# Performance work log

Hardware: AMD Instinct MI355X
Metric: run time of the kernel (lower is better)

The kernel has to match this reference:

```python
import jax, jax.numpy as jnp
import numpy as np
import math

H = 16
D_MODEL = 1024
D_K = D_MODEL // H  # 64
B = 4
S = 2048
D_V = 64


def setup_inputs() -> dict:
    key0 = jax.random.key(0)
    ks = jax.random.split(key0, 7)
    scale = 1.0 / math.sqrt(D_MODEL)
    return {
        "query": jax.random.normal(ks[0], (B, S, D_MODEL), jnp.float32),
        "key": jax.random.normal(ks[1], (B, S, D_MODEL), jnp.float32),
        "value": jax.random.normal(ks[2], (B, D_V, S), jnp.float32),
        "Wq": jax.random.normal(ks[3], (D_MODEL, D_MODEL), jnp.float32) * scale,
        "bq": jax.random.normal(ks[4], (D_MODEL,), jnp.float32) * scale,
        "Wk": jax.random.normal(ks[5], (D_MODEL, D_MODEL), jnp.float32) * scale,
        "bk": jax.random.normal(ks[6], (D_MODEL,), jnp.float32) * scale,
    }


def reference(query, key, value, Wq, bq, Wk, bk):
    nb = query.shape[0]
    # Linear projections then split heads: [B,S,d_model] -> [B,h,S,d_k]
    q = (query @ Wq.T + bq).reshape(nb, -1, H, D_K).transpose(0, 2, 1, 3)
    k = (key @ Wk.T + bk).reshape(nb, -1, H, D_K).transpose(0, 2, 1, 3)
    # value.repeat(h,1,1,1).permute(1,0,3,2): [B,dv,Sk] -> broadcast over heads
    # with last two axes swapped -> effectively v[b,s,d] = value[b,d,s]
    v = jnp.swapaxes(value, 1, 2)  # [B, Sk, dv]
    # Scaled dot-product attention (mask branch is a no-op: m == zeros)
    scores = jnp.einsum("bhqd,bhkd->bhqk", q, k) / math.sqrt(D_K)
    p_attn = jax.nn.softmax(scores, axis=-1)
    # value identical across heads, contract directly with base v
    x = jnp.einsum("bhqk,bkd->bhqd", p_attn, v)  # [B,h,Sq,dv]
    return (jnp.mean(x, axis=1), q)
```

## Files before the change

kernel.cpp:

```cpp
#include <hip/hip_runtime.h>


typedef unsigned short u16;
typedef __attribute__((ext_vector_type(8))) u16 u16x8;
typedef __attribute__((ext_vector_type(8))) __bf16 bf16x8;
typedef __attribute__((ext_vector_type(4))) float f32x4;
typedef __attribute__((ext_vector_type(16))) float f32x16;
typedef __attribute__((ext_vector_type(2))) unsigned u32x2;
typedef __attribute__((ext_vector_type(4))) unsigned u32x4;

typedef const __attribute__((address_space(1))) void gvoid;
typedef __attribute__((address_space(3))) void lvoid;

__device__ __forceinline__ void gload16(const void* g, void* l) {
  __builtin_amdgcn_global_load_lds((gvoid*)g, (lvoid*)l, 16, 0, 0);
}

__device__ __forceinline__ u16 f2bf(float f) {
  unsigned u = __builtin_bit_cast(unsigned, f);
  u += 0x7fffu + ((u >> 16) & 1u);
  return (u16)(u >> 16);
}

__device__ __forceinline__ unsigned cvtpk(float lo, float hi) {
  unsigned r;
  asm("v_cvt_pk_bf16_f32 %0, %1, %2" : "=v"(r) : "v"(lo), "v"(hi));
  return r;
}

__device__ __forceinline__ float exp2a(float x) {
  float r;
  asm("v_exp_f32 %0, %1" : "=v"(r) : "v"(x));
  return r;
}

__device__ __forceinline__ f32x16 zero16() {
  f32x16 z;
#pragma unroll
  for (int i = 0; i < 16; ++i) z[i] = 0.f;
  return z;
}

__global__ void cvt_small(const float* __restrict__ wq, const float* __restrict__ wk,
                          const float* __restrict__ v,
                          u16* __restrict__ wqb, u16* __restrict__ wkb, u16* __restrict__ vb) {
  int i = blockIdx.x * 256 + threadIdx.x;
  const float* s;
  u16* d;
  int off;
  if (i < 262144)      { s = wq; d = wqb; off = i; }
  else if (i < 524288) { s = wk; d = wkb; off = i - 262144; }
  else if (i < 655360) { s = v;  d = vb;  off = i - 524288; }
  else return;
  float4 x = reinterpret_cast<const float4*>(s)[off];
  ushort4 o;
  o.x = f2bf(x.x); o.y = f2bf(x.y); o.z = f2bf(x.z); o.w = f2bf(x.w);
  reinterpret_cast<ushort4*>(d)[off] = o;
}

__global__ __launch_bounds__(256) void proj_gemm(
    const float* __restrict__ qf, const float* __restrict__ kf,
    const u16* __restrict__ Wqb, const u16* __restrict__ Wkb,
    const float* __restrict__ bq, const float* __restrict__ bk,
    float* __restrict__ out1, u16* __restrict__ k_ws)
{
  const int z = blockIdx.z;
  const float* __restrict__ A = z ? kf : qf;
  const u16* __restrict__ W = z ? Wkb : Wqb;
  const float* __restrict__ bias = z ? bk : bq;

  __shared__ u16 As[2][128 * 64];
  __shared__ u16 Bs[2][128 * 64];

  const int tid = threadIdx.x;
  const int lane = tid & 63;
  const int w = tid >> 6;
  const int ln = lane & 15;
  const int lh = lane >> 4;
  const int wm = w >> 1, wn = w & 1;
  const int n0 = blockIdx.x * 128;
  const int j0 = blockIdx.y * 128;

  f32x4 acc[4][4];
#pragma unroll
  for (int mt = 0; mt < 4; ++mt)
#pragma unroll
    for (int nt = 0; nt < 4; ++nt)
      acc[mt][nt] = f32x4{0.f, 0.f, 0.f, 0.f};

  const int r_ = tid >> 3, c8_ = tid & 7;

#pragma unroll
  for (int it = 0; it < 4; ++it) {
    int r = it * 32 + r_;
    gload16(&W[(size_t)(j0 + r) * 1024 + c8_ * 8], &Bs[0][(it * 256 + w * 64) * 8]);
  }
#pragma unroll
  for (int j = 0; j < 4; ++j) {
    int u = tid + j * 256;
    int r = u >> 3, c8 = (u & 7) * 8;
    const float* s = &A[(size_t)(n0 + r) * 1024 + c8];
    float4 x0 = *reinterpret_cast<const float4*>(s);
    float4 x1 = *reinterpret_cast<const float4*>(s + 4);
    u32x4 wv{cvtpk(x0.x, x0.y), cvtpk(x0.z, x0.w), cvtpk(x1.x, x1.y), cvtpk(x1.z, x1.w)};
    *reinterpret_cast<u32x4*>(&As[0][r * 64 + c8]) = wv;
  }
  __syncthreads();

  for (int kt = 0; kt < 16; ++kt) {
    const int cur = kt & 1, nb = cur ^ 1;
    float4 ax0[4], ax1[4];
    if (kt < 15) {
#pragma unroll
      for (int it = 0; it < 4; ++it) {
        int r = it * 32 + r_;
        gload16(&W[(size_t)(j0 + r) * 1024 + (kt + 1) * 64 + c8_ * 8],
                &Bs[nb][(it * 256 + w * 64) * 8]);
      }
#pragma unroll
      for (int j = 0; j < 4; ++j) {
        int u = tid + j * 256;
        int r = u >> 3, c8 = (u & 7) * 8;
        const float* s = &A[(size_t)(n0 + r) * 1024 + (kt + 1) * 64 + c8];
        ax0[j] = *reinterpret_cast<const float4*>(s);
        ax1[j] = *reinterpret_cast<const float4*>(s + 4);
      }
    }
#pragma unroll
    for (int ks = 0; ks < 2; ++ks) {
      bf16x8 a[4], bfr[4];
#pragma unroll
      for (int mt = 0; mt < 4; ++mt)
        a[mt] = __builtin_bit_cast(bf16x8,
            *reinterpret_cast<const u16x8*>(&As[cur][(wm * 64 + mt * 16 + ln) * 64 + lh * 8 + ks * 32]));
#pragma unroll
      for (int nt = 0; nt < 4; ++nt)
        bfr[nt] = __builtin_bit_cast(bf16x8,
            *reinterpret_cast<const u16x8*>(&Bs[cur][(wn * 64 + nt * 16 + ln) * 64 + lh * 8 + ks * 32]));
      __builtin_amdgcn_s_setprio(1);
#pragma unroll
      for (int mt = 0; mt < 4; ++mt)
#pragma unroll
        for (int nt = 0; nt < 4; ++nt)
          acc[mt][nt] = __builtin_amdgcn_mfma_f32_16x16x32_bf16(a[mt], bfr[nt], acc[mt][nt], 0, 0, 0);
      __builtin_amdgcn_s_setprio(0);
    }
    if (kt < 15) {
#pragma unroll
      for (int j = 0; j < 4; ++j) {
        int u = tid + j * 256;
        int r = u >> 3, c8 = (u & 7) * 8;
        u32x4 wv{cvtpk(ax0[j].x, ax0[j].y), cvtpk(ax0[j].z, ax0[j].w),
                 cvtpk(ax1[j].x, ax1[j].y), cvtpk(ax1[j].z, ax1[j].w)};
        *reinterpret_cast<u32x4*>(&As[nb][r * 64 + c8]) = wv;
      }
      __syncthreads();
    }
  }

#pragma unroll
  for (int nt = 0; nt < 4; ++nt) {
    int j = j0 + wn * 64 + nt * 16 + ln;
    float bv = bias[j];
    int h = j >> 6, d = j & 63;
#pragma unroll
    for (int mt = 0; mt < 4; ++mt) {
#pragma unroll
      for (int r = 0; r < 4; ++r) {
        int n = n0 + wm * 64 + mt * 16 + lh * 4 + r;
        int bidx = n >> 11, s = n & 2047;
        size_t off = ((size_t)(bidx * 16 + h) * 2048 + s) * 64 + d;
        float val = acc[mt][nt][r] + bv;
        if (z == 0) out1[off] = val;
        else        k_ws[off] = f2bf(val);
      }
    }
  }
}

#define SOFTMAX_CVT(P, PF0, PF1, LACC)                                               \
  {                                                                                  \
    _Pragma("unroll")                                                                \
    for (int r = 0; r < 16; ++r) P[r] = exp2a(P[r]);                                 \
    LACC += (((P[0]+P[1])+(P[2]+P[3])) + ((P[4]+P[5])+(P[6]+P[7])))                  \
          + (((P[8]+P[9])+(P[10]+P[11])) + ((P[12]+P[13])+(P[14]+P[15])));           \
    u32x2 sA0 = __builtin_amdgcn_permlane32_swap(cvtpk(P[0],P[1]),   cvtpk(P[4],P[5]),   false,false); \
    u32x2 sB0 = __builtin_amdgcn_permlane32_swap(cvtpk(P[2],P[3]),   cvtpk(P[6],P[7]),   false,false); \
    u32x2 sA1 = __builtin_amdgcn_permlane32_swap(cvtpk(P[8],P[9]),   cvtpk(P[12],P[13]), false,false); \
    u32x2 sB1 = __builtin_amdgcn_permlane32_swap(cvtpk(P[10],P[11]), cvtpk(P[14],P[15]), false,false); \
    u32x4 w0_{sA0[0], sB0[0], sA0[1], sB0[1]};                                       \
    u32x4 w1_{sA1[0], sB1[0], sA1[1], sB1[1]};                                       \
    PF0 = __builtin_bit_cast(bf16x8, w0_);                                           \
    PF1 = __builtin_bit_cast(bf16x8, w1_);                                           \
  }

#define ST_BLOCK(ST)                                                                 \
  {                                                                                  \
    f32x16 p = zero16();                                                             \
    __builtin_amdgcn_s_setprio(1);                                                   \
    _Pragma("unroll")                                                                \
    for (int c = 0; c < 4; ++c) {                                                    \
      int ka = bo + ((((ST * 32 + l31) * 128) + c * 32 + hi * 16) ^ xm);             \
      bf16x8 kf = __builtin_bit_cast(bf16x8, *reinterpret_cast<const u16x8*>(KtB + ka)); \
      p = __builtin_amdgcn_mfma_f32_32x32x16_bf16(kf, aq[c], p, 0, 0, 0);            \
    }                                                                                \
    __builtin_amdgcn_s_setprio(0);                                                   \
    bf16x8 pf0, pf1;                                                                 \
    SOFTMAX_CVT(p, pf0, pf1, lA);                                                    \
    _Pragma("unroll")                                                                \
    for (int kc = 0; kc < 2; ++kc) {                                                 \
      int cb = ST * 64 + kc * 32 + hi * 16;                                          \
      bf16x8 vA = __builtin_bit_cast(bf16x8,                                         \
          *reinterpret_cast<const u16x8*>(VtB + bo + ((l31 * 128 + cb) ^ xm)));      \
      bf16x8 vB = __builtin_bit_cast(bf16x8,                                         \
          *reinterpret_cast<const u16x8*>(VtB + bo + (((32 + l31) * 128 + cb) ^ xm))); \
      bf16x8 pf = kc ? pf1 : pf0;                                                    \
      __builtin_amdgcn_s_setprio(1);                                                 \
      oA = __builtin_amdgcn_mfma_f32_32x32x16_bf16(vA, pf, oA, 0, 0, 0);             \
      oB = __builtin_amdgcn_mfma_f32_32x32x16_bf16(vB, pf, oB, 0, 0, 0);             \
      __builtin_amdgcn_s_setprio(0);                                                 \
    }                                                                                \
  }

__global__ __launch_bounds__(256, 4) void attn_kernel(
    const float* __restrict__ qf, const u16* __restrict__ k_ws,
    const u16* __restrict__ valb, u16* __restrict__ x_ws)
{
  const int wgid = (blockIdx.x & 7) * 128 + (blockIdx.x >> 3);
  const int qblk = wgid & 15;
  const int h = (wgid >> 4) & 15;
  const int b = wgid >> 8;
  const int bh = b * 16 + h;

  const int tid = threadIdx.x, lane = tid & 63, w = tid >> 6;
  const int l31 = lane & 31, hi = lane >> 5;
  const int xm = (lane & 7) << 4;

  __shared__ u16 Kt[2][4096];
  __shared__ u16 Vt[2][4096];
  char* KtB = (char*)&Kt[0][0];
  char* VtB = (char*)&Vt[0][0];

  bf16x8 aq[4];
  {
    const float qs = 0.125f * 1.4426950408889634f;
    const size_t qb0 = ((size_t)bh * 2048 + qblk * 128 + w * 32 + l31) * 64;
#pragma unroll
    for (int c = 0; c < 4; ++c) {
      const float* src = &qf[qb0 + c * 16 + hi * 8];
      float4 v0 = *reinterpret_cast<const float4*>(src);
      float4 v1 = *reinterpret_cast<const float4*>(src + 4);
      u16x8 t;
      t[0] = f2bf(v0.x * qs); t[1] = f2bf(v0.y * qs);
      t[2] = f2bf(v0.z * qs); t[3] = f2bf(v0.w * qs);
      t[4] = f2bf(v1.x * qs); t[5] = f2bf(v1.y * qs);
      t[6] = f2bf(v1.z * qs); t[7] = f2bf(v1.w * qs);
      aq[c] = __builtin_bit_cast(bf16x8, t);
    }
  }

  const u16* kg = k_ws + (size_t)bh * 131072;
  const u16* vg = valb + (size_t)b * 131072;
  const int u0 = tid, u1 = tid + 256;
  const u16* ks0 = kg + (u0 >> 3) * 64 + ((u0 ^ (u0 >> 3)) & 7) * 8;
  const u16* ks1 = kg + (u1 >> 3) * 64 + ((u1 ^ (u1 >> 3)) & 7) * 8;
  const u16* vs0 = vg + (u0 >> 3) * 2048 + ((u0 ^ (u0 >> 3)) & 7) * 8;
  const u16* vs1 = vg + (u1 >> 3) * 2048 + ((u1 ^ (u1 >> 3)) & 7) * 8;
  u16* kd0 = &Kt[0][(w * 64) * 8];
  u16* kd1 = &Kt[0][(256 + w * 64) * 8];
  u16* vd0 = &Vt[0][(w * 64) * 8];
  u16* vd1 = &Vt[0][(256 + w * 64) * 8];

  gload16(ks0, kd0); gload16(ks1, kd1);
  gload16(vs0, vd0); gload16(vs1, vd1);

  float lA = 0.0f;
  f32x16 oA = zero16(), oB = zero16();
  int cur = 0;
  __syncthreads();

  for (int t = 0; t < 32; ++t) {
    if (t < 31) {
      int nb = (cur ^ 1) * 4096;
      size_t ko = (size_t)(t + 1) * 4096;
      int vo = (t + 1) * 64;
      gload16(ks0 + ko, kd0 + nb); gload16(ks1 + ko, kd1 + nb);
      gload16(vs0 + vo, vd0 + nb); gload16(vs1 + vo, vd1 + nb);
    }
    const int bo = cur * 8192;

    ST_BLOCK(0)
    ST_BLOCK(1)

    __syncthreads();
    cur ^= 1;
  }

  float lr = lA + __shfl_xor(lA, 32);
  float inv = 1.0f / lr;
  size_t ob0 = ((size_t)bh * 2048 + qblk * 128 + w * 32 + l31) * 64;
#pragma unroll
  for (int g = 0; g < 4; ++g) {
    u32x2 aa{cvtpk(oA[g*4+0]*inv, oA[g*4+1]*inv), cvtpk(oA[g*4+2]*inv, oA[g*4+3]*inv)};
    u32x2 bb{cvtpk(oB[g*4+0]*inv, oB[g*4+1]*inv), cvtpk(oB[g*4+2]*inv, oB[g*4+3]*inv)};
    *reinterpret_cast<u32x2*>(&x_ws[ob0 + g * 8 + hi * 4]) = aa;
    *reinterpret_cast<u32x2*>(&x_ws[ob0 + 32 + g * 8 + hi * 4]) = bb;
  }
}

__global__ void mean_heads(const u16* __restrict__ x_ws, float* __restrict__ out0) {
  int i = blockIdx.x * 256 + threadIdx.x;
  int d0 = (i & 7) * 8;
  int s = (i >> 3) & 2047;
  int b = i >> 14;
  float acc[8];
#pragma unroll
  for (int j = 0; j < 8; ++j) acc[j] = 0.f;
#pragma unroll
  for (int h = 0; h < 16; ++h) {
    u16x8 v = *reinterpret_cast<const u16x8*>(
        &x_ws[(((size_t)(b * 16 + h) * 2048 + s) << 6) + d0]);
#pragma unroll
    for (int j = 0; j < 8; ++j)
      acc[j] += __builtin_bit_cast(float, (unsigned)v[j] << 16);
  }
  float4 o0{acc[0] * 0.0625f, acc[1] * 0.0625f, acc[2] * 0.0625f, acc[3] * 0.0625f};
  float4 o1{acc[4] * 0.0625f, acc[5] * 0.0625f, acc[6] * 0.0625f, acc[7] * 0.0625f};
  size_t ob = ((size_t)(b * 2048 + s) << 6) + d0;
  *reinterpret_cast<float4*>(&out0[ob]) = o0;
  *reinterpret_cast<float4*>(&out0[ob + 4]) = o1;
}

extern "C" void kernel_launch(void* const* d_in, const int* in_sizes, int n_in,
                              void* d_out, int out_size, void* d_ws, size_t ws_size,
                              hipStream_t stream) {
  (void)in_sizes; (void)n_in; (void)out_size; (void)ws_size;
  const float* query = (const float*)d_in[0];
  const float* key   = (const float*)d_in[1];
  const float* value = (const float*)d_in[2];
  const float* Wq    = (const float*)d_in[3];
  const float* bq    = (const float*)d_in[4];
  const float* Wk    = (const float*)d_in[5];
  const float* bk    = (const float*)d_in[6];

  float* out0 = (float*)d_out;
  float* out1 = out0 + 524288;

  char* ws = (char*)d_ws;
  const size_t MB = 1u << 20;
  u16* x_ws = (u16*)(ws + 0);
  u16* Wqb  = (u16*)(ws + 32 * MB);
  u16* Wkb  = (u16*)(ws + 34 * MB);
  u16* valb = (u16*)(ws + 36 * MB);
  u16* k_ws = (u16*)(ws + 37 * MB);

  cvt_small<<<2560, 256, 0, stream>>>(Wq, Wk, value, Wqb, Wkb, valb);
  proj_gemm<<<dim3(64, 8, 2), 256, 0, stream>>>(query, key, Wqb, Wkb, bq, bk, out1, k_ws);
  attn_kernel<<<1024, 256, 0, stream>>>(out1, k_ws, valb, x_ws);
  mean_heads<<<256, 256, 0, stream>>>(x_ws, out0);
}
```

Measured before the change: 154.7 us.

## Load projection A operand straight into registers and swizzle the weight tile in LDS

The fp32 activation tile is no longer staged and converted through shared memory. Each lane now loads its MFMA fragment directly from global memory and converts it to bf16 in registers, which removes the As buffer and its LDS writes. The weight tile in LDS gets an XOR swizzle on its 16-byte chunks to reduce bank conflicts on fragment reads. The trade-off is that the activation loads are no longer prefetched a stage ahead: they are issued just before the MFMAs and fetched redundantly by the two column-warps, so memory latency may be exposed.

```diff
diff --git a/kernel.cpp b/kernel.cpp
--- a/kernel.cpp
+++ b/kernel.cpp
@@ -69,7 +69,6 @@
   const u16* __restrict__ W = z ? Wkb : Wqb;
   const float* __restrict__ bias = z ? bk : bq;
 
-  __shared__ u16 As[2][128 * 64];
   __shared__ u16 Bs[2][128 * 64];
 
   const int tid = threadIdx.x;
@@ -88,55 +87,43 @@
     for (int nt = 0; nt < 4; ++nt)
       acc[mt][nt] = f32x4{0.f, 0.f, 0.f, 0.f};
 
-  const int r_ = tid >> 3, c8_ = tid & 7;
-
-#pragma unroll
-  for (int it = 0; it < 4; ++it) {
-    int r = it * 32 + r_;
-    gload16(&W[(size_t)(j0 + r) * 1024 + c8_ * 8], &Bs[0][(it * 256 + w * 64) * 8]);
-  }
-#pragma unroll
-  for (int j = 0; j < 4; ++j) {
-    int u = tid + j * 256;
-    int r = u >> 3, c8 = (u & 7) * 8;
-    const float* s = &A[(size_t)(n0 + r) * 1024 + c8];
-    float4 x0 = *reinterpret_cast<const float4*>(s);
-    float4 x1 = *reinterpret_cast<const float4*>(s + 4);
-    u32x4 wv{cvtpk(x0.x, x0.y), cvtpk(x0.z, x0.w), cvtpk(x1.x, x1.y), cvtpk(x1.z, x1.w)};
-    *reinterpret_cast<u32x4*>(&As[0][r * 64 + c8]) = wv;
-  }
+  const int r_ = tid >> 3;
+  const int swz = (tid & 7) ^ (r_ & 7);
+  const float* Abase = A + (size_t)(n0 + wm * 64 + ln) * 1024 + lh * 8;
+  const int bxm = (ln & 7) << 4;
+  char* BsB = (char*)&Bs[0][0];
+
+#pragma unroll
+  for (int it = 0; it < 4; ++it)
+    gload16(&W[(size_t)(j0 + it * 32 + r_) * 1024 + swz * 8], &Bs[0][(it * 256 + w * 64) * 8]);
   __syncthreads();
 
   for (int kt = 0; kt < 16; ++kt) {
     const int cur = kt & 1, nb = cur ^ 1;
-    float4 ax0[4], ax1[4];
     if (kt < 15) {
 #pragma unroll
-      for (int it = 0; it < 4; ++it) {
-        int r = it * 32 + r_;
-        gload16(&W[(size_t)(j0 + r) * 1024 + (kt + 1) * 64 + c8_ * 8],
+      for (int it = 0; it < 4; ++it)
+        gload16(&W[(size_t)(j0 + it * 32 + r_) * 1024 + (kt + 1) * 64 + swz * 8],
                 &Bs[nb][(it * 256 + w * 64) * 8]);
+    }
+#pragma unroll
+    for (int ks = 0; ks < 2; ++ks) {
+      bf16x8 a[4];
+#pragma unroll
+      for (int mt = 0; mt < 4; ++mt) {
+        const float* s = Abase + (size_t)mt * 16 * 1024 + kt * 64 + ks * 32;
+        float4 x0 = *reinterpret_cast<const float4*>(s);
+        float4 x1 = *reinterpret_cast<const float4*>(s + 4);
+        u32x4 wv{cvtpk(x0.x, x0.y), cvtpk(x0.z, x0.w), cvtpk(x1.x, x1.y), cvtpk(x1.z, x1.w)};
+        a[mt] = __builtin_bit_cast(bf16x8, wv);
       }
-#pragma unroll
-      for (int j = 0; j < 4; ++j) {
-        int u = tid + j * 256;
-        int r = u >> 3, c8 = (u & 7) * 8;
-        const float* s = &A[(size_t)(n0 + r) * 1024 + (kt + 1) * 64 + c8];
-        ax0[j] = *reinterpret_cast<const float4*>(s);
-        ax1[j] = *reinterpret_cast<const float4*>(s + 4);
+      bf16x8 bfr[4];
+#pragma unroll
+      for (int nt = 0; nt < 4; ++nt) {
+        int row = wn * 64 + nt * 16 + ln;
+        int ba = cur * 16384 + row * 128 + ((lh * 16 + ks * 64) ^ bxm);
+        bfr[nt] = __builtin_bit_cast(bf16x8, *reinterpret_cast<const u16x8*>(BsB + ba));
       }
-    }
-#pragma unroll
-    for (int ks = 0; ks < 2; ++ks) {
-      bf16x8 a[4], bfr[4];
-#pragma unroll
-      for (int mt = 0; mt < 4; ++mt)
-        a[mt] = __builtin_bit_cast(bf16x8,
-            *reinterpret_cast<const u16x8*>(&As[cur][(wm * 64 + mt * 16 + ln) * 64 + lh * 8 + ks * 32]));
-#pragma unroll
-      for (int nt = 0; nt < 4; ++nt)
-        bfr[nt] = __builtin_bit_cast(bf16x8,
-            *reinterpret_cast<const u16x8*>(&Bs[cur][(wn * 64 + nt * 16 + ln) * 64 + lh * 8 + ks * 32]));
       __builtin_amdgcn_s_setprio(1);
 #pragma unroll
       for (int mt = 0; mt < 4; ++mt)
@@ -145,17 +132,7 @@
           acc[mt][nt] = __builtin_amdgcn_mfma_f32_16x16x32_bf16(a[mt], bfr[nt], acc[mt][nt], 0, 0, 0);
       __builtin_amdgcn_s_setprio(0);
     }
-    if (kt < 15) {
-#pragma unroll
-      for (int j = 0; j < 4; ++j) {
-        int u = tid + j * 256;
-        int r = u >> 3, c8 = (u & 7) * 8;
-        u32x4 wv{cvtpk(ax0[j].x, ax0[j].y), cvtpk(ax0[j].z, ax0[j].w),
-                 cvtpk(ax1[j].x, ax1[j].y), cvtpk(ax1[j].z, ax1[j].w)};
-        *reinterpret_cast<u32x4*>(&As[nb][r * 64 + c8]) = wv;
-      }
-      __syncthreads();
-    }
+    __syncthreads();
   }
 
 #pragma unroll
```

Result: slower. 230.3 us (+48.9%).
